# Kernel optimization log

Measured on AMD Instinct MI355X. Metric: run time of the kernel, lower is better.

Reference implementation:

```python
import jax, jax.numpy as jnp
import numpy as np

# Model dims (see init_kwargs)
NU = 4096   # num_users (one-hot feature dim)
NV = 4096   # num_items
C = 5       # num_classes (rating levels)
H0 = 256    # hidden[0]
H1 = 128    # hidden[1]
D_IN = 512  # input_dim (side-feature dense dim)
SIDE = 1024 # raw side-feature dim (u_features.size(1))
NB = 2      # nb basis matrices in bilinear decoder


def setup_inputs() -> dict:
    key = jax.random.key(0)
    ks = jax.random.split(key, 16)
    u = jax.random.randint(ks[0], (4096,), 0, NU)
    v = jax.random.randint(ks[1], (4096,), 0, NV)
    r = jax.random.randint(ks[2], (4096,), 0, C)  # unused by forward (as in source)
    raw = jax.random.randint(ks[3], (NU, NV), 0, 4 * C)
    adj_matrix = (raw[None, :, :] == jnp.arange(1, C + 1)[:, None, None]).astype(jnp.float32)
    u_features = jax.random.normal(ks[4], (NU, SIDE), jnp.float32)
    v_features = jax.random.normal(ks[5], (NV, SIDE), jnp.float32)
    def w(k, shape, fan):
        return jax.random.normal(k, shape, jnp.float32) / np.float32(np.sqrt(fan))
    u_w = w(ks[6], (C, NU, H0), NU)          # per-relation GraphConvolution user weights
    v_w = w(ks[7], (C, NV, H0), NV)          # per-relation item weights
    Wu1 = w(ks[8], (D_IN, SIDE), SIDE); bu1 = jnp.zeros((D_IN,), jnp.float32)
    Wv1 = w(ks[9], (D_IN, SIDE), SIDE); bv1 = jnp.zeros((D_IN,), jnp.float32)
    Wu2 = w(ks[10], (H1, D_IN + H0), D_IN + H0)
    Wv2 = w(ks[11], (H1, D_IN + H0), D_IN + H0)
    P = w(ks[12], (NB, H1, H1), H1)          # bilinear basis matrices
    a = w(ks[13], (NB, C), NB)               # basis -> class coefficients
    return dict(u=u, v=v, r=r, adj_matrix=adj_matrix, u_features=u_features,
                v_features=v_features, u_w=u_w, v_w=v_w, Wu1=Wu1, bu1=bu1,
                Wv1=Wv1, bv1=bv1, Wu2=Wu2, Wv2=Wv2, P=P, a=a)


def reference(u, v, r, adj_matrix, u_features, v_features, u_w, v_w,
              Wu1, bu1, Wv1, bv1, Wu2, Wv2, P, a):
    # m = adj[:, u][:, :, v]  -> [C, nu, nv]
    m = adj_matrix[:, u][:, :, v]
    # degree normalization exactly as written in gc_encoder
    du = jnp.abs(m.sum(axis=1).sum(axis=0))   # [nv]
    di = jnp.abs(m.sum(axis=2).sum(axis=0))   # [nu]
    c = 1.0 / jnp.concatenate([du, di], axis=0)
    c = jnp.where(jnp.isinf(c), jnp.zeros_like(c), c)
    # ordinal weight sharing: W_r = sum_{s<=r} Theta_s; one-hot feat @ W == gather rows
    cu = jnp.cumsum(u_w, axis=0)              # [C, NU, H0]
    cv = jnp.cumsum(v_w, axis=0)
    u_x = cu[:, u]                            # [C, nu, H0]
    v_x = cv[:, v]                            # [C, nv, H0]
    # accumulate per-relation message passing across all C relations at once
    u_next = jnp.einsum('ruv,rvh->uh', m, v_x)   # [nu, H0]
    v_next = jnp.einsum('ruv,ruh->vh', m, u_x)   # [nv, H0]
    z = jax.nn.relu(jnp.concatenate([u_next, v_next], axis=0) * c[:, None])
    nu = u.shape[0]
    u_z, v_z = z[:nu], z[nu:]
    u_f = jax.nn.relu(u_features[u] @ Wu1.T + bu1)
    v_f = jax.nn.relu(v_features[v] @ Wv1.T + bv1)
    u_h = jax.nn.relu(jnp.concatenate([u_z, u_f], axis=1) @ Wu2.T)   # [nu, H1]
    v_h = jax.nn.relu(jnp.concatenate([v_z, v_f], axis=1) @ Wv2.T)   # [nv, H1]
    # bilinear mixture decoder: logits[c,u,v] = sum_b a[b,c] * u_h Q_b v_h^T
    outputs = jnp.einsum('ud,bde,ve,bc->cuv', u_h, P, v_h, a)        # [C, nu, nv]
    logp = jax.nn.log_softmax(outputs, axis=0)
    prob = jnp.exp(logp)
    ratings = jnp.arange(1, C + 1, dtype=outputs.dtype)
    m_hat = jnp.einsum('c,cuv->uv', ratings, prob)
    # losses over observed entries
    mask = m.sum(axis=0) > 0
    n_obs = jnp.maximum(mask.sum(), 1).astype(outputs.dtype)
    loss = -(m * logp).sum() / n_obs
    target = (jnp.argmax(m, axis=0) + 1).astype(outputs.dtype)
    se = jnp.where(mask, (m_hat - target) ** 2, jnp.zeros_like(m_hat))
    rmse_loss = jnp.sqrt(se.sum() / n_obs)
    return (m_hat, loss, rmse_loss)
```

## Files before the change

kernel.cpp:

```cpp
#include <hip/hip_runtime.h>
#include <stdint.h>

#define N4   4096
#define H0   256
#define SIDE 1024
#define DIN  512
#define HCAT 768
#define H1   128
#define NC   5
#define NUV  16777216ULL
#define CAP  1536

typedef __attribute__((ext_vector_type(8))) short short8;
typedef __attribute__((ext_vector_type(4))) float floatx4;

__device__ __forceinline__ unsigned short f2bf(float f) {
    unsigned int u;
    __builtin_memcpy(&u, &f, 4);
    unsigned int r = (u + 0x7FFFu + ((u >> 16) & 1u)) >> 16;
    return (unsigned short)r;
}

__device__ __forceinline__ float bf2f(unsigned short b) {
    unsigned int u = (unsigned int)b << 16;
// ... 41 lines not shown
    int b = blockIdx.x, t = threadIdx.x;
    if (b < 4096) {
        int bx = b & 63, by = b >> 6;
        int row = t >> 2;
        int seg = (t & 3) * 16;
        int p0 = by * 64, q0 = bx * 64;
        uint4 vdat = *(const uint4*)(code + (size_t)(p0 + row) * N4 + q0 + seg);
        *(uint4*)(&tile[row][seg]) = vdat;
        __syncthreads();
        union { uint4 u4; uint8_t bb[16]; } o;
        #pragma unroll
        for (int l = 0; l < 16; l++) o.bb[l] = tile[seg + l][row];
        *(uint4*)(codeT + (size_t)(q0 + row) * N4 + p0 + seg) = o.u4;
    } else {
        int node = (b - 4096) & 4095;
        int side = (b - 4096) >> 12;
        const float* w = side ? v_w : u_w;
        const int* cnt = side ? cnt_v : cnt_u;
        unsigned short* out = side ? T_Bv : T_Au;
        int h = t;
        float c = (float)cnt[node];
        float acc = 0.f;
        #pragma unroll
        for (int r = 0; r < NC; r++) {
            size_t idx = ((size_t)r * N4 + node) * H0 + h;
            acc += w[idx];
            union { _Float16 h16; unsigned short s; } cvt;
            cvt.h16 = (_Float16)(acc * c);
            out[idx] = cvt.s;
        }
    }
}

__global__ __launch_bounds__(256) void k_compactF(const uint8_t* __restrict__ code,
                                                  const uint8_t* __restrict__ codeT,
                                                  const int* __restrict__ cnt_u,
                                                  const int* __restrict__ cnt_v,
                                                  unsigned short* __restrict__ idxU,
                                                  int* __restrict__ nnzU,
                                                  float* __restrict__ rowDeg,
                                                  unsigned short* __restrict__ idxV,
                                                  int* __restrict__ nnzV,
                                                  float* __restrict__ colDeg) {
    __shared__ float cw[4096];
    __shared__ int wtot[4];
    __shared__ float wdeg[4];
    __shared__ __align__(16) unsigned short ebuf[CAP];
    int side = blockIdx.y;
    const uint8_t* codeRows = side ? codeT : code;
    const int* cntOther = side ? cnt_u : cnt_v;
    unsigned short* idx = side ? idxV : idxU;
    int* nnz = side ? nnzV : nnzU;
    float* deg = side ? colDeg : rowDeg;

    int p = blockIdx.x, t = threadIdx.x;
    int lane = t & 63, wv = t >> 6;
    const int4* co4 = (const int4*)cntOther;
    #pragma unroll
    for (int l = 0; l < 4; l++) {
        int4 ci = co4[t + l * 256];
        ((float4*)cw)[t + l * 256] =
            make_float4((float)ci.x, (float)ci.y, (float)ci.z, (float)ci.w);
    }
    uint4 w = ((const uint4*)(codeRows + (size_t)p * N4))[t];
    unsigned char b[16];
    __builtin_memcpy(b, &w, 16);
    int cnt = 0;
    #pragma unroll
    for (int j = 0; j < 16; j++) cnt += (b[j] != 0);
    int sc = cnt;
    #pragma unroll
    for (int off = 1; off < 64; off <<= 1) {
        int up = __shfl_up(sc, off, 64);
        if (lane >= off) sc += up;
    }
    if (lane == 63) wtot[wv] = sc;
    __syncthreads();
    int wbase = 0;
    #pragma unroll
    for (int ww = 0; ww < 4; ww++) wbase += (ww < wv) ? wtot[ww] : 0;
    int total = wtot[0] + wtot[1] + wtot[2] + wtot[3];
    int pos = wbase + sc - cnt;
    float dsum = 0.f;
    #pragma unroll
    for (int j = 0; j < 16; j++) {
        int r = b[j];
        if (r) {
            int q = t * 16 + j;
            if (pos < CAP) ebuf[pos] = (unsigned short)((r - 1) * N4 + q);
            pos++;
            dsum += cw[q];
        }
    }
    #pragma unroll
    for (int off = 32; off; off >>= 1) dsum += __shfl_down(dsum, off, 64);
    if (lane == 0) wdeg[wv] = dsum;
    __syncthreads();
    int tw = total < CAP ? total : CAP;
    if (t == 0) { deg[p] = wdeg[0] + wdeg[1] + wdeg[2] + wdeg[3]; nnz[p] = tw; }
    for (int e = t; e < tw; e += 256) idx[(size_t)p * CAP + e] = ebuf[e];
}

__global__ __launch_bounds__(256) void k_gatherE(const unsigned short* __restrict__ idxU,
                                                 const int* __restrict__ nnzU,
                                                 const unsigned short* __restrict__ T_Bv,
                                                 const unsigned short* __restrict__ idxV,
                                                 const int* __restrict__ nnzV,
                                                 const unsigned short* __restrict__ T_Au,
                                                 float* __restrict__ pnn) {
    __shared__ __align__(16) unsigned short sidx[CAP];
    __shared__ float red[16][132];
    __shared__ int sbnd[2];
    int bid = blockIdx.x;
    int side  = bid >> 15;
    int r1    = bid & 32767;
    int epoch = r1 >> 13;
    int r2    = r1 & 8191;
    int p     = r2 >> 1;
    int half  = r2 & 1;

    const unsigned short* idx = side ? idxV : idxU;
    const int* nnz = side ? nnzV : nnzU;
    const char* tb = (const char*)(side ? T_Au : T_Bv);

    int t = threadIdx.x;
    int n = nnz[p];
    const unsigned short* rowIdx = idx + (size_t)p * CAP;
    int nv = (n + 7) >> 3;
    for (int i = t; i < nv; i += 256)
        ((uint4*)sidx)[i] = ((const uint4*)rowIdx)[i];
    __syncthreads();
    if (t < 2) {
        int target = (epoch + t) << 10;
// ... 26 lines not shown
        union { uint4 u; _Float16 h[8]; } cv;
        cv.u = d0;
        #pragma unroll
        for (int k = 0; k < 8; k++) acc[k] += (float)cv.h[k];
        cv.u = d1;
        #pragma unroll
        for (int k = 0; k < 8; k++) acc[k] += (float)cv.h[k];
        cv.u = d2;
        #pragma unroll
        for (int k = 0; k < 8; k++) acc[k] += (float)cv.h[k];
        cv.u = d3;
        #pragma unroll
        for (int k = 0; k < 8; k++) acc[k] += (float)cv.h[k];
    }
    for (int e = nmain + s; e < ehi; e += 16) {
        int o = ((int)sidx[e]) << 9;
        uint4 d = *(const uint4*)(tb + o + boff);
        union { uint4 u; _Float16 h[8]; } cv;
        cv.u = d;
        #pragma unroll
        for (int k = 0; k < 8; k++) acc[k] += (float)cv.h[k];
    }
    #pragma unroll
    for (int k = 0; k < 8; k++) red[s][c * 8 + k] = acc[k];
    __syncthreads();
    if (t < 128) {
        float sum = 0.f;
        #pragma unroll
        for (int ss = 0; ss < 16; ss++) sum += red[ss][t];
        pnn[(((size_t)(side * 4 + epoch)) * N4 + p) * H0 + half * 128 + t] = sum;
    }
}

__global__ __launch_bounds__(256) void k_fuse1(const uint8_t* __restrict__ code,
                                               const int* __restrict__ u,
                                               const int* __restrict__ v,
                                               uint8_t* __restrict__ codeR,
                                               const float* __restrict__ pnn,
                                               const float* __restrict__ colDeg,
                                               const float* __restrict__ rowDeg,
                                               unsigned short* __restrict__ chiU,
                                               unsigned short* __restrict__ cloU,
                                               unsigned short* __restrict__ chiV,
                                               unsigned short* __restrict__ cloV,
                                               const float* __restrict__ u_feat,
                                               unsigned short* __restrict__ fuhi,
                                               unsigned short* __restrict__ fulo,
                                               const float* __restrict__ v_feat,
                                               unsigned short* __restrict__ fvhi,
                                               unsigned short* __restrict__ fvlo,
                                               const float* __restrict__ Wu1,
                                               unsigned short* __restrict__ wuhi,
                                               unsigned short* __restrict__ wulo,
                                               const float* __restrict__ Wv1,
                                               unsigned short* __restrict__ wvhi,
                                               unsigned short* __restrict__ wvlo,
                                               const float* __restrict__ Wu2,
                                               unsigned short* __restrict__ w2uhi,
                                               unsigned short* __restrict__ w2ulo,
                                               const float* __restrict__ Wv2,
                                               unsigned short* __restrict__ w2vhi,
                                               unsigned short* __restrict__ w2vlo,
                                               const float* __restrict__ P,
                                               float* __restrict__ Pt) {
    __shared__ __align__(16) uint8_t rowbuf[4096];
    int b = blockIdx.x, t = threadIdx.x;
    if (b < 4096) {
        int i = b;
        int urow = u[i];
        ((uint4*)rowbuf)[t] = ((const uint4*)(code + (size_t)urow * N4))[t];
        __syncthreads();
        uint8_t ob[16];
        #pragma unroll
        for (int w = 0; w < 4; w++) {
            int4 vv = ((const int4*)v)[t * 4 + w];
            ob[w * 4 + 0] = rowbuf[vv.x];
            ob[w * 4 + 1] = rowbuf[vv.y];
            ob[w * 4 + 2] = rowbuf[vv.z];
            ob[w * 4 + 3] = rowbuf[vv.w];
        }
        uint4 o;
        __builtin_memcpy(&o, ob, 16);
        ((uint4*)(codeR + (size_t)i * N4))[t] = o;
        return;
    }
    if (b < 12288) {
        int i = (b - 4096) & 4095;
        int side = (b - 4096) >> 12;
        const int* idxs = side ? v : u;
        const int* idxo = side ? u : v;
        const float* deg = side ? rowDeg : colDeg;
        unsigned short* catHi = side ? chiV : chiU;
        unsigned short* catLo = side ? cloV : cloU;
        int h = t;
        float d = deg[idxo[i]];
        float inv = d > 0.f ? 1.f / d : 0.f;
        int row = idxs[i];
        const float* pr = pnn + ((size_t)side * 4 * N4 + row) * H0 + h;
        float nnv = 0.f;
        #pragma unroll
        for (int e = 0; e < 4; e++) nnv += pr[(size_t)e * N4 * H0];
        float val = fmaxf(nnv * inv, 0.f);
        unsigned short hb = f2bf(val);
        catHi[(size_t)i * HCAT + h] = hb;
        catLo[(size_t)i * HCAT + h] = f2bf(val - bf2f(hb));
        return;
    }
    if (b >= 21696) {
        int tid = (b - 21696) * 256 + t;
        int bb = tid >> 14;
        int d = (tid >> 7) & 127;
        int e = tid & 127;
        Pt[((size_t)bb * 128 + e) * 128 + d] = P[tid];
        return;
    }
    const float* src;
    unsigned short* hi;
    unsigned short* lo;
    int lb;
    if (b < 16384)      { src = u_feat; hi = fuhi; lo = fulo; lb = b - 12288; }
    else if (b < 20480) { src = v_feat; hi = fvhi; lo = fvlo; lb = b - 16384; }
    else if (b < 20992) { src = Wu1; hi = wuhi; lo = wulo; lb = b - 20480; }
    else if (b < 21504) { src = Wv1; hi = wvhi; lo = wvlo; lb = b - 20992; }
    else if (b < 21600) { src = Wu2; hi = w2uhi; lo = w2ulo; lb = b - 21504; }
    else                { src = Wv2; hi = w2vhi; lo = w2vlo; lb = b - 21600; }
    size_t g = ((size_t)lb * 256 + t) * 4;
    float4 x = *(const float4*)(src + g);
    float f[4] = {x.x, x.y, x.z, x.w};
    unsigned short hh[4], ll[4];
    #pragma unroll
    for (int k = 0; k < 4; k++) {
        unsigned short hb = f2bf(f[k]);
        hh[k] = hb;
        ll[k] = f2bf(f[k] - bf2f(hb));
    }
    *(ushort4*)(hi + g) = make_ushort4(hh[0], hh[1], hh[2], hh[3]);
    *(ushort4*)(lo + g) = make_ushort4(ll[0], ll[1], ll[2], ll[3]);
}

__global__ __launch_bounds__(256) void k_l1F(const unsigned short* __restrict__ fuhi,
                                             const unsigned short* __restrict__ fulo,
                                             const unsigned short* __restrict__ fvhi,
                                             const unsigned short* __restrict__ fvlo,
                                             const int* __restrict__ u,
                                             const int* __restrict__ v,
                                             const unsigned short* __restrict__ wuhi,
                                             const unsigned short* __restrict__ wulo,
                                             const unsigned short* __restrict__ wvhi,
                                             const unsigned short* __restrict__ wvlo,
                                             const float* __restrict__ bu1,
                                             const float* __restrict__ bv1,
                                             unsigned short* __restrict__ chiU,
                                             unsigned short* __restrict__ cloU,
                                             unsigned short* __restrict__ chiV,
                                             unsigned short* __restrict__ cloV) {
    __shared__ __align__(16) unsigned short Bh[64][72];
    __shared__ __align__(16) unsigned short Bl[64][72];
    int side = blockIdx.z;
    const unsigned short* Ahi = side ? fvhi : fuhi;
    const unsigned short* Alo = side ? fvlo : fulo;
    const int* rowmap = side ? v : u;
    const unsigned short* Bhi = side ? wvhi : wuhi;
    const unsigned short* Blo = side ? wvlo : wulo;
    const float* bias = side ? bv1 : bu1;
    unsigned short* CHi = (side ? chiV : chiU) + H0;
    unsigned short* CLo = (side ? cloV : cloU) + H0;

    int t = threadIdx.x;
    int wave = t >> 6, lane = t & 63;
    int lr = lane & 15;
    int lk = lane >> 4;
    int i0 = blockIdx.y * 64 + wave * 16;
    int n0 = blockIdx.x * 64;
    int gi = rowmap[i0 + lr];
    const unsigned short* pah = Ahi + (size_t)gi * SIDE;
    const unsigned short* pal = Alo + (size_t)gi * SIDE;
    int srow = t >> 2, sseg = (t & 3) * 16;
    floatx4 acc[4];
    #pragma unroll
    for (int jt = 0; jt < 4; jt++) acc[jt] = (floatx4){0.f, 0.f, 0.f, 0.f};
    for (int ks = 0; ks < SIDE / 64; ks++) {
        const unsigned short* sh = Bhi + (size_t)(n0 + srow) * SIDE + ks * 64 + sseg;
        const unsigned short* sl = Blo + (size_t)(n0 + srow) * SIDE + ks * 64 + sseg;
        __syncthreads();
        *(uint4*)(&Bh[srow][sseg]) = *(const uint4*)sh;
        *(uint4*)(&Bh[srow][sseg + 8]) = *(const uint4*)(sh + 8);
        *(uint4*)(&Bl[srow][sseg]) = *(const uint4*)sl;
        *(uint4*)(&Bl[srow][sseg + 8]) = *(const uint4*)(sl + 8);
        __syncthreads();
        #pragma unroll
        for (int kk = 0; kk < 2; kk++) {
            int ko = ks * 64 + kk * 32 + lk * 8;
            short8 ah = *(const short8*)(pah + ko);
            short8 al = *(const short8*)(pal + ko);
            #pragma unroll
            for (int jt = 0; jt < 4; jt++) {
                short8 bh = *(const short8*)(&Bh[jt * 16 + lr][kk * 32 + lk * 8]);
                short8 bl = *(const short8*)(&Bl[jt * 16 + lr][kk * 32 + lk * 8]);
                acc[jt] = __builtin_amdgcn_mfma_f32_16x16x32_bf16(ah, bh, acc[jt], 0, 0, 0);
                acc[jt] = __builtin_amdgcn_mfma_f32_16x16x32_bf16(ah, bl, acc[jt], 0, 0, 0);
                acc[jt] = __builtin_amdgcn_mfma_f32_16x16x32_bf16(al, bh, acc[jt], 0, 0, 0);
            }
        }
    }
    #pragma unroll
    for (int jt = 0; jt < 4; jt++) {
        int cn = n0 + jt * 16 + lr;
        float bb = bias[cn];
        #pragma unroll
        for (int r = 0; r < 4; r++) {
            int ci = i0 + lk * 4 + r;
            float vv = fmaxf(acc[jt][r] + bb, 0.f);
            unsigned short hb = f2bf(vv);
            CHi[(size_t)ci * HCAT + cn] = hb;
            CLo[(size_t)ci * HCAT + cn] = f2bf(vv - bf2f(hb));
        }
    }
}

__global__ __launch_bounds__(256) void k_l2F(const unsigned short* __restrict__ chiU,
                                             const unsigned short* __restrict__ cloU,
                                             const unsigned short* __restrict__ w2uhi,
                                             const unsigned short* __restrict__ w2ulo,
                                             float* __restrict__ uh,
                                             const unsigned short* __restrict__ chiV,
                                             const unsigned short* __restrict__ cloV,
                                             const unsigned short* __restrict__ w2vhi,
                                             const unsigned short* __restrict__ w2vlo,
                                             unsigned short* __restrict__ vhb) {
    __shared__ __align__(16) unsigned short Bh[64][72];
    __shared__ __align__(16) unsigned short Bl[64][72];
    int side = blockIdx.z;
    const unsigned short* Ahi = side ? chiV : chiU;
    const unsigned short* Alo = side ? cloV : cloU;
    const unsigned short* Bhi = side ? w2vhi : w2uhi;
    const unsigned short* Blo = side ? w2vlo : w2ulo;

    int t = threadIdx.x;
    int wave = t >> 6, lane = t & 63;
    int lr = lane & 15;
    int lk = lane >> 4;
    int i0 = blockIdx.y * 64 + wave * 16;
    int n0 = blockIdx.x * 64;
    const unsigned short* pah = Ahi + (size_t)(i0 + lr) * HCAT;
    const unsigned short* pal = Alo + (size_t)(i0 + lr) * HCAT;
    int srow = t >> 2, sseg = (t & 3) * 16;
    floatx4 acc[4];
    #pragma unroll
    for (int jt = 0; jt < 4; jt++) acc[jt] = (floatx4){0.f, 0.f, 0.f, 0.f};
    for (int ks = 0; ks < HCAT / 64; ks++) {
        const unsigned short* sh = Bhi + (size_t)(n0 + srow) * HCAT + ks * 64 + sseg;
        const unsigned short* sl = Blo + (size_t)(n0 + srow) * HCAT + ks * 64 + sseg;
        __syncthreads();
        *(uint4*)(&Bh[srow][sseg]) = *(const uint4*)sh;
        *(uint4*)(&Bh[srow][sseg + 8]) = *(const uint4*)(sh + 8);
        *(uint4*)(&Bl[srow][sseg]) = *(const uint4*)sl;
        *(uint4*)(&Bl[srow][sseg + 8]) = *(const uint4*)(sl + 8);
        __syncthreads();
        #pragma unroll
        for (int kk = 0; kk < 2; kk++) {
            int ko = ks * 64 + kk * 32 + lk * 8;
            short8 ah = *(const short8*)(pah + ko);
            short8 al = *(const short8*)(pal + ko);
            #pragma unroll
            for (int jt = 0; jt < 4; jt++) {
                short8 bh = *(const short8*)(&Bh[jt * 16 + lr][kk * 32 + lk * 8]);
                short8 bl = *(const short8*)(&Bl[jt * 16 + lr][kk * 32 + lk * 8]);
                acc[jt] = __builtin_amdgcn_mfma_f32_16x16x32_bf16(ah, bh, acc[jt], 0, 0, 0);
                acc[jt] = __builtin_amdgcn_mfma_f32_16x16x32_bf16(ah, bl, acc[jt], 0, 0, 0);
                acc[jt] = __builtin_amdgcn_mfma_f32_16x16x32_bf16(al, bh, acc[jt], 0, 0, 0);
            }
        }
    }
    #pragma unroll
    for (int jt = 0; jt < 4; jt++) {
        int cn = n0 + jt * 16 + lr;
        #pragma unroll
        for (int r = 0; r < 4; r++) {
            int ci = i0 + lk * 4 + r;
            float vv = fmaxf(acc[jt][r], 0.f);
            if (side) {
                vhb[(size_t)ci * H1 + cn] = f2bf(vv);
            } else {
                uh[(size_t)ci * H1 + cn] = vv;
            }
        }
    }
}

template <int TM, int TN, int BK, int RM, int RN>
__global__ __launch_bounds__(256) void k_gemm(const float* __restrict__ A, int lda,
                                              const float* __restrict__ B, int ldb,
                                              float* __restrict__ C, int ldc, int K,
                                              size_t bzs, size_t czs) {
    constexpr int TX = TN / RN;
    constexpr int TY = TM / RM;
    static_assert(TX * TY == 256, "block must be 256");
    __shared__ float As[BK][TM + 4];
    __shared__ float Bs[BK][TN + 4];
    int tid = threadIdx.x;
    int tx = tid % TX, ty = tid / TX;
    int i0 = blockIdx.x * TM, n0 = blockIdx.y * TN;
    const float* Bz = B + (size_t)blockIdx.z * bzs;
    float acc[RM][RN] = {};
    for (int k0 = 0; k0 < K; k0 += BK) {
        for (int g = tid; g < TM * BK / 4; g += 256) {
            int i = g / (BK / 4), kc = g % (BK / 4);
            float4 val = *(const float4*)(A + (size_t)(i0 + i) * lda + k0 + kc * 4);
            As[kc * 4 + 0][i] = val.x; As[kc * 4 + 1][i] = val.y;
            As[kc * 4 + 2][i] = val.z; As[kc * 4 + 3][i] = val.w;
        }
        for (int g = tid; g < TN * BK / 4; g += 256) {
            int n = g / (BK / 4), kc = g % (BK / 4);
            float4 val = *(const float4*)(Bz + (size_t)(n0 + n) * ldb + k0 + kc * 4);
            Bs[kc * 4 + 0][n] = val.x; Bs[kc * 4 + 1][n] = val.y;
            Bs[kc * 4 + 2][n] = val.z; Bs[kc * 4 + 3][n] = val.w;
        }
        __syncthreads();
        #pragma unroll
        for (int k = 0; k < BK; k++) {
            float av[RM], bv[RN];
            #pragma unroll
            for (int m = 0; m < RM; m++) av[m] = As[k][ty * RM + m];
            #pragma unroll
            for (int n = 0; n < RN; n++) bv[n] = Bs[k][tx * RN + n];
            #pragma unroll
            for (int m = 0; m < RM; m++)
                #pragma unroll
                for (int n = 0; n < RN; n++)
                    acc[m][n] = fmaf(av[m], bv[n], acc[m][n]);
        }
        __syncthreads();
    }
    #pragma unroll
    for (int m = 0; m < RM; m++) {
        int ig = i0 + ty * RM + m;
        #pragma unroll
        for (int n = 0; n < RN; n++) {
            unsigned short* Cz16 = (unsigned short*)C + (size_t)blockIdx.z * czs;
            Cz16[(size_t)ig * ldc + n0 + tx * RN + n] = f2bf(acc[m][n]);
        }
    }
}

__global__ __launch_bounds__(256) void k_scores3(const unsigned short* __restrict__ tb,
                                                 const unsigned short* __restrict__ vhb,
                                                 const uint8_t* __restrict__ codeR,
                                                 const float* __restrict__ a_f,
                                                 float* __restrict__ mhat,
                                                 float* __restrict__ part) {
    __shared__ float wred[4][3];
    int t = threadIdx.x;
    int wave = t >> 6, lane = t & 63;
    int lr = lane & 15;
    int lk = lane >> 4;
    int i0 = blockIdx.y * 64 + wave * 16;
    int j0 = blockIdx.x * 128;
    float sa0[NC], sa1[NC];
    #pragma unroll
    for (int c = 0; c < NC; c++) { sa0[c] = a_f[c]; sa1[c] = a_f[5 + c]; }

    const unsigned short* t0p = tb;
    const unsigned short* t1p = tb + (size_t)N4 * H1;
    short8 a0[4], a1[4];
    #pragma unroll
    for (int kc = 0; kc < 4; kc++) {
        size_t off = (size_t)(i0 + lr) * H1 + kc * 32 + lk * 8;
        a0[kc] = *(const short8*)(t0p + off);
        a1[kc] = *(const short8*)(t1p + off);
    }

    const uint8_t* crbase = codeR + (size_t)(i0 + lk * 4) * N4 + lr;
    short8 bcur[4];
// ... 126 lines not shown
    const float* bu1    = (const float*)d_in[9];
    const float* Wv1    = (const float*)d_in[10];
    const float* bv1    = (const float*)d_in[11];
    const float* Wu2    = (const float*)d_in[12];
    const float* Wv2    = (const float*)d_in[13];
    const float* P      = (const float*)d_in[14];
    const float* a      = (const float*)d_in[15];
    float* out = (float*)d_out;

    char* ws = (char*)d_ws;
    const size_t O_CODE  = 0;
    const size_t O_CNTU  = 16777216;
    const size_t O_CNTV  = O_CNTU + 16384;
    const size_t O_ACC   = O_CNTV + 16384;
    const size_t O_TAU   = O_ACC + 256;
    const size_t O_TBV   = O_TAU + 10485760;
    const size_t O_IDXU  = O_TBV + 10485760;
    const size_t O_IDXV  = O_IDXU + 12582912;
    const size_t O_NNZU  = O_IDXV + 12582912;
    const size_t O_NNZV  = O_NNZU + 16384;
    const size_t O_RDEG  = O_NNZV + 16384;
    const size_t O_CDEG  = O_RDEG + 16384;
    const size_t O_UNN   = O_CDEG + 16384;
    const size_t O_VNN   = O_UNN + 4194304;
    const size_t O_UCAT  = O_VNN + 4194304;
    const size_t O_VCAT  = O_UCAT + 12582912;
    const size_t O_UH    = O_VCAT + 12582912;
    const size_t O_VHB   = O_UH + 2097152;
    const size_t O_PT    = O_VHB + 1048576;
    const size_t O_TB    = O_PT + 131072;
    const size_t O_CODET = O_UCAT;
    const size_t O_CODER = O_TAU;
    const size_t O_PART  = O_CNTU;
    const size_t O_FUHI  = O_IDXU;
    const size_t O_FULO  = O_IDXV;
    const size_t O_CHIU  = O_UCAT;
    const size_t O_CLOU  = O_UCAT + 6291456;
    const size_t O_CHIV  = O_VCAT;
    const size_t O_CLOV  = O_VCAT + 6291456;
    const size_t S_FVHI  = 0;
    const size_t S_FVLO  = 8388608;
    const size_t S_WUHI  = 16777216;
    const size_t S_WULO  = S_WUHI + 1048576;
    const size_t S_WVHI  = S_WULO + 1048576;
    const size_t S_WVLO  = S_WVHI + 1048576;
    const size_t S_W2UHI = S_WVLO + 1048576;
    const size_t S_W2ULO = S_W2UHI + 196608;
    const size_t S_W2VHI = S_W2ULO + 196608;
    const size_t S_W2VLO = S_W2VHI + 196608;
    const size_t S_PNN   = 25165824;

    uint8_t* code  = (uint8_t*)(ws + O_CODE);
    uint8_t* codeT = (uint8_t*)(ws + O_CODET);
    uint8_t* codeR = (uint8_t*)(ws + O_CODER);
    int* cnt_u = (int*)(ws + O_CNTU);
    int* cnt_v = (int*)(ws + O_CNTV);
    unsigned short* T_Au = (unsigned short*)(ws + O_TAU);
    unsigned short* T_Bv = (unsigned short*)(ws + O_TBV);
    unsigned short* idxU = (unsigned short*)(ws + O_IDXU);
    unsigned short* idxV = (unsigned short*)(ws + O_IDXV);
    int* nnzU = (int*)(ws + O_NNZU);
    int* nnzV = (int*)(ws + O_NNZV);
    float* rowDeg = (float*)(ws + O_RDEG);
    float* colDeg = (float*)(ws + O_CDEG);
    float* uh = (float*)(ws + O_UH);
    unsigned short* vhb = (unsigned short*)(ws + O_VHB);
    float* Pt = (float*)(ws + O_PT);
    unsigned short* tb = (unsigned short*)(ws + O_TB);
    float* part = (float*)(ws + O_PART);
    unsigned short* fuhi = (unsigned short*)(ws + O_FUHI);
    unsigned short* fulo = (unsigned short*)(ws + O_FULO);
    unsigned short* chiU = (unsigned short*)(ws + O_CHIU);
    unsigned short* cloU = (unsigned short*)(ws + O_CLOU);
    unsigned short* chiV = (unsigned short*)(ws + O_CHIV);
    unsigned short* cloV = (unsigned short*)(ws + O_CLOV);
    char* outc = (char*)d_out;
    unsigned short* fvhi = (unsigned short*)(outc + S_FVHI);
    unsigned short* fvlo = (unsigned short*)(outc + S_FVLO);
    unsigned short* wuhi = (unsigned short*)(outc + S_WUHI);
    unsigned short* wulo = (unsigned short*)(outc + S_WULO);
    unsigned short* wvhi = (unsigned short*)(outc + S_WVHI);
    unsigned short* wvlo = (unsigned short*)(outc + S_WVLO);
    unsigned short* w2uhi = (unsigned short*)(outc + S_W2UHI);
    unsigned short* w2ulo = (unsigned short*)(outc + S_W2ULO);
    unsigned short* w2vhi = (unsigned short*)(outc + S_W2VHI);
    unsigned short* w2vlo = (unsigned short*)(outc + S_W2VLO);
    float* pnn = (float*)(outc + S_PNN);

    hipMemsetAsync(ws + O_CNTU, 0, 16384 + 16384, stream);

    k_codeF<<<16400, 256, 0, stream>>>(adj, (uchar4*)code, u, v, cnt_u, cnt_v);
    k_fuse0<<<12288, 256, 0, stream>>>(code, codeT, u_w, cnt_u, T_Au, v_w, cnt_v, T_Bv);
    k_compactF<<<dim3(N4, 2), 256, 0, stream>>>(code, codeT, cnt_u, cnt_v,
                                                idxU, nnzU, rowDeg, idxV, nnzV, colDeg);
    k_gatherE<<<65536, 256, 0, stream>>>(idxU, nnzU, T_Bv, idxV, nnzV, T_Au, pnn);
    k_fuse1<<<21824, 256, 0, stream>>>(code, u, v, codeR, pnn, colDeg, rowDeg,
                                       chiU, cloU, chiV, cloV,
                                       u_feat, fuhi, fulo,
                                       v_feat, fvhi, fvlo,
                                       Wu1, wuhi, wulo, Wv1, wvhi, wvlo,
                                       Wu2, w2uhi, w2ulo, Wv2, w2vhi, w2vlo,
                                       P, Pt);
    k_l1F<<<dim3(8, 64, 2), 256, 0, stream>>>(fuhi, fulo, fvhi, fvlo, u, v,
                                              wuhi, wulo, wvhi, wvlo, bu1, bv1,
                                              chiU, cloU, chiV, cloV);
    k_l2F<<<dim3(2, 64, 2), 256, 0, stream>>>(chiU, cloU, w2uhi, w2ulo, uh,
                                              chiV, cloV, w2vhi, w2vlo, vhb);
    k_gemm<64, 32, 16, 4, 2>
        <<<dim3(64, 4, 2), 256, 0, stream>>>(uh, H1, Pt, H1,
                                             (float*)tb, H1, H1,
                                             (size_t)H1 * H1, (size_t)N4 * H1);
    k_scores3<<<dim3(32, 64), 256, 0, stream>>>(tb, vhb, codeR, a, out, part);
    k_finalize<<<1, 256, 0, stream>>>(part, out);
}
```

Before: 881.8 us.

## Fuse prep conversions into compaction, merge z-build into layer1, MFMA the Pt GEMM

New measurement: 874.0 us. Within noise of the previous version (-0.9%).

```diff
diff --git a/kernel.cpp b/kernel.cpp
--- a/kernel.cpp
+++ b/kernel.cpp
@@ -97,73 +97,132 @@
     }
 }
 
-__global__ __launch_bounds__(256) void k_compactF(const uint8_t* __restrict__ code,
-                                                  const uint8_t* __restrict__ codeT,
-                                                  const int* __restrict__ cnt_u,
-                                                  const int* __restrict__ cnt_v,
-                                                  unsigned short* __restrict__ idxU,
-                                                  int* __restrict__ nnzU,
-                                                  float* __restrict__ rowDeg,
-                                                  unsigned short* __restrict__ idxV,
-                                                  int* __restrict__ nnzV,
-                                                  float* __restrict__ colDeg) {
+__global__ __launch_bounds__(256) void k_prep(const uint8_t* __restrict__ code,
+                                              const uint8_t* __restrict__ codeT,
+                                              const int* __restrict__ cnt_u,
+                                              const int* __restrict__ cnt_v,
+                                              unsigned short* __restrict__ idxU,
+                                              int* __restrict__ nnzU,
+                                              float* __restrict__ rowDeg,
+                                              unsigned short* __restrict__ idxV,
+                                              int* __restrict__ nnzV,
+                                              float* __restrict__ colDeg,
+                                              const float* __restrict__ u_feat,
+                                              unsigned short* __restrict__ fuhi,
+                                              unsigned short* __restrict__ fulo,
+                                              const float* __restrict__ v_feat,
+                                              unsigned short* __restrict__ fvhi,
+                                              unsigned short* __restrict__ fvlo,
+                                              const float* __restrict__ Wu1,
+                                              unsigned short* __restrict__ wuhi,
+                                              unsigned short* __restrict__ wulo,
+                                              const float* __restrict__ Wv1,
+                                              unsigned short* __restrict__ wvhi,
+                                              unsigned short* __restrict__ wvlo,
+                                              const float* __restrict__ Wu2,
+                                              unsigned short* __restrict__ w2uhi,
+                                              unsigned short* __restrict__ w2ulo,
+                                              const float* __restrict__ Wv2,
+                                              unsigned short* __restrict__ w2vhi,
+                                              unsigned short* __restrict__ w2vlo,
+                                              const float* __restrict__ P,
+                                              unsigned short* __restrict__ pthi,
+                                              unsigned short* __restrict__ ptlo) {
     __shared__ float cw[4096];
     __shared__ int wtot[4];
     __shared__ float wdeg[4];
     __shared__ __align__(16) unsigned short ebuf[CAP];
-    int side = blockIdx.y;
-    const uint8_t* codeRows = side ? codeT : code;
-    const int* cntOther = side ? cnt_u : cnt_v;
-    unsigned short* idx = side ? idxV : idxU;
-    int* nnz = side ? nnzV : nnzU;
-    float* deg = side ? colDeg : rowDeg;
-
-    int p = blockIdx.x, t = threadIdx.x;
-    int lane = t & 63, wv = t >> 6;
-    const int4* co4 = (const int4*)cntOther;
-    #pragma unroll
-    for (int l = 0; l < 4; l++) {
-        int4 ci = co4[t + l * 256];
-        ((float4*)cw)[t + l * 256] =
-            make_float4((float)ci.x, (float)ci.y, (float)ci.z, (float)ci.w);
-    }
-    uint4 w = ((const uint4*)(codeRows + (size_t)p * N4))[t];
-    unsigned char b[16];
-    __builtin_memcpy(b, &w, 16);
-    int cnt = 0;
-    #pragma unroll
-    for (int j = 0; j < 16; j++) cnt += (b[j] != 0);
-    int sc = cnt;
-    #pragma unroll
-    for (int off = 1; off < 64; off <<= 1) {
-        int up = __shfl_up(sc, off, 64);
-        if (lane >= off) sc += up;
-    }
-    if (lane == 63) wtot[wv] = sc;
-    __syncthreads();
-    int wbase = 0;
-    #pragma unroll
-    for (int ww = 0; ww < 4; ww++) wbase += (ww < wv) ? wtot[ww] : 0;
-    int total = wtot[0] + wtot[1] + wtot[2] + wtot[3];
-    int pos = wbase + sc - cnt;
-    float dsum = 0.f;
-    #pragma unroll
-    for (int j = 0; j < 16; j++) {
-        int r = b[j];
-        if (r) {
-            int q = t * 16 + j;
-            if (pos < CAP) ebuf[pos] = (unsigned short)((r - 1) * N4 + q);
-            pos++;
-            dsum += cw[q];
-        }
-    }
-    #pragma unroll
-    for (int off = 32; off; off >>= 1) dsum += __shfl_down(dsum, off, 64);
-    if (lane == 0) wdeg[wv] = dsum;
-    __syncthreads();
-    int tw = total < CAP ? total : CAP;
-    if (t == 0) { deg[p] = wdeg[0] + wdeg[1] + wdeg[2] + wdeg[3]; nnz[p] = tw; }
-    for (int e = t; e < tw; e += 256) idx[(size_t)p * CAP + e] = ebuf[e];
+    int b = blockIdx.x, t = threadIdx.x;
+    if (b < 8192) {
+        int side = b >> 12;
+        int p = b & 4095;
+        const uint8_t* codeRows = side ? codeT : code;
+        const int* cntOther = side ? cnt_u : cnt_v;
+        unsigned short* idx = side ? idxV : idxU;
+        int* nnz = side ? nnzV : nnzU;
+        float* deg = side ? colDeg : rowDeg;
+
+        int lane = t & 63, wv = t >> 6;
+        const int4* co4 = (const int4*)cntOther;
+        #pragma unroll
+        for (int l = 0; l < 4; l++) {
+            int4 ci = co4[t + l * 256];
+            ((float4*)cw)[t + l * 256] =
+                make_float4((float)ci.x, (float)ci.y, (float)ci.z, (float)ci.w);
+        }
+        uint4 w = ((const uint4*)(codeRows + (size_t)p * N4))[t];
+        unsigned char bb[16];
+        __builtin_memcpy(bb, &w, 16);
+        int cnt = 0;
+        #pragma unroll
+        for (int j = 0; j < 16; j++) cnt += (bb[j] != 0);
+        int sc = cnt;
+        #pragma unroll
+        for (int off = 1; off < 64; off <<= 1) {
+            int up = __shfl_up(sc, off, 64);
+            if (lane >= off) sc += up;
+        }
+        if (lane == 63) wtot[wv] = sc;
+        __syncthreads();
+        int wbase = 0;
+        #pragma unroll
+        for (int ww = 0; ww < 4; ww++) wbase += (ww < wv) ? wtot[ww] : 0;
+        int total = wtot[0] + wtot[1] + wtot[2] + wtot[3];
+        int pos = wbase + sc - cnt;
+        float dsum = 0.f;
+        #pragma unroll
+        for (int j = 0; j < 16; j++) {
+            int r = bb[j];
+            if (r) {
+                int q = t * 16 + j;
+                if (pos < CAP) ebuf[pos] = (unsigned short)((r - 1) * N4 + q);
+                pos++;
+                dsum += cw[q];
+            }
+        }
+        #pragma unroll
+        for (int off = 32; off; off >>= 1) dsum += __shfl_down(dsum, off, 64);
+        if (lane == 0) wdeg[wv] = dsum;
+        __syncthreads();
+        int tw = total < CAP ? total : CAP;
+        if (t == 0) { deg[p] = wdeg[0] + wdeg[1] + wdeg[2] + wdeg[3]; nnz[p] = tw; }
+        for (int e = t; e < tw; e += 256) idx[(size_t)p * CAP + e] = ebuf[e];
+        return;
+    }
+    if (b >= 17600) {
+        int tid = (b - 17600) * 256 + t;
+        int bb = tid >> 14;
+        int d = (tid >> 7) & 127;
+        int e = tid & 127;
+        float val = P[tid];
+        unsigned short hb = f2bf(val);
+        size_t o = ((size_t)bb * 128 + e) * 128 + d;
+        pthi[o] = hb;
+        ptlo[o] = f2bf(val - bf2f(hb));
+        return;
+    }
+    const float* src;
+    unsigned short* hi;
+    unsigned short* lo;
+    int lb;
+    if (b < 12288)      { src = u_feat; hi = fuhi; lo = fulo; lb = b - 8192; }
+    else if (b < 16384) { src = v_feat; hi = fvhi; lo = fvlo; lb = b - 12288; }
+    else if (b < 16896) { src = Wu1; hi = wuhi; lo = wulo; lb = b - 16384; }
+    else if (b < 17408) { src = Wv1; hi = wvhi; lo = wvlo; lb = b - 16896; }
+    else if (b < 17504) { src = Wu2; hi = w2uhi; lo = w2ulo; lb = b - 17408; }
+    else                { src = Wv2; hi = w2vhi; lo = w2vlo; lb = b - 17504; }
+    size_t g = ((size_t)lb * 256 + t) * 4;
+    float4 x = *(const float4*)(src + g);
+    float f[4] = {x.x, x.y, x.z, x.w};
+    unsigned short hh[4], ll[4];
+    #pragma unroll
+    for (int k = 0; k < 4; k++) {
+        unsigned short hb = f2bf(f[k]);
+        hh[k] = hb;
+        ll[k] = f2bf(f[k] - bf2f(hb));
+    }
+    *(ushort4*)(hi + g) = make_ushort4(hh[0], hh[1], hh[2], hh[3]);
+    *(ushort4*)(lo + g) = make_ushort4(ll[0], ll[1], ll[2], ll[3]);
 }
 
 __global__ __launch_bounds__(256) void k_gatherE(const unsigned short* __restrict__ idxU,
@@ -256,113 +315,7 @@
     }
 }
 
-__global__ __launch_bounds__(256) void k_fuse1(const uint8_t* __restrict__ code,
-                                               const int* __restrict__ u,
-                                               const int* __restrict__ v,
-                                               uint8_t* __restrict__ codeR,
-                                               const float* __restrict__ pnn,
-                                               const float* __restrict__ colDeg,
-                                               const float* __restrict__ rowDeg,
-                                               unsigned short* __restrict__ chiU,
-                                               unsigned short* __restrict__ cloU,
-                                               unsigned short* __restrict__ chiV,
-                                               unsigned short* __restrict__ cloV,
-                                               const float* __restrict__ u_feat,
-                                               unsigned short* __restrict__ fuhi,
-                                               unsigned short* __restrict__ fulo,
-                                               const float* __restrict__ v_feat,
-                                               unsigned short* __restrict__ fvhi,
-                                               unsigned short* __restrict__ fvlo,
-                                               const float* __restrict__ Wu1,
-                                               unsigned short* __restrict__ wuhi,
-                                               unsigned short* __restrict__ wulo,
-                                               const float* __restrict__ Wv1,
-                                               unsigned short* __restrict__ wvhi,
-                                               unsigned short* __restrict__ wvlo,
-                                               const float* __restrict__ Wu2,
-                                               unsigned short* __restrict__ w2uhi,
-                                               unsigned short* __restrict__ w2ulo,
-                                               const float* __restrict__ Wv2,
-                                               unsigned short* __restrict__ w2vhi,
-                                               unsigned short* __restrict__ w2vlo,
-                                               const float* __restrict__ P,
-                                               float* __restrict__ Pt) {
-    __shared__ __align__(16) uint8_t rowbuf[4096];
-    int b = blockIdx.x, t = threadIdx.x;
-    if (b < 4096) {
-        int i = b;
-        int urow = u[i];
-        ((uint4*)rowbuf)[t] = ((const uint4*)(code + (size_t)urow * N4))[t];
-        __syncthreads();
-        uint8_t ob[16];
-        #pragma unroll
-        for (int w = 0; w < 4; w++) {
-            int4 vv = ((const int4*)v)[t * 4 + w];
-            ob[w * 4 + 0] = rowbuf[vv.x];
-            ob[w * 4 + 1] = rowbuf[vv.y];
-            ob[w * 4 + 2] = rowbuf[vv.z];
-            ob[w * 4 + 3] = rowbuf[vv.w];
-        }
-        uint4 o;
-        __builtin_memcpy(&o, ob, 16);
-        ((uint4*)(codeR + (size_t)i * N4))[t] = o;
-        return;
-    }
-    if (b < 12288) {
-        int i = (b - 4096) & 4095;
-        int side = (b - 4096) >> 12;
-        const int* idxs = side ? v : u;
-        const int* idxo = side ? u : v;
-        const float* deg = side ? rowDeg : colDeg;
-        unsigned short* catHi = side ? chiV : chiU;
-        unsigned short* catLo = side ? cloV : cloU;
-        int h = t;
-        float d = deg[idxo[i]];
-        float inv = d > 0.f ? 1.f / d : 0.f;
-        int row = idxs[i];
-        const float* pr = pnn + ((size_t)side * 4 * N4 + row) * H0 + h;
-        float nnv = 0.f;
-        #pragma unroll
-        for (int e = 0; e < 4; e++) nnv += pr[(size_t)e * N4 * H0];
-        float val = fmaxf(nnv * inv, 0.f);
-        unsigned short hb = f2bf(val);
-        catHi[(size_t)i * HCAT + h] = hb;
-        catLo[(size_t)i * HCAT + h] = f2bf(val - bf2f(hb));
-        return;
-    }
-    if (b >= 21696) {
-        int tid = (b - 21696) * 256 + t;
-        int bb = tid >> 14;
-        int d = (tid >> 7) & 127;
-        int e = tid & 127;
-        Pt[((size_t)bb * 128 + e) * 128 + d] = P[tid];
-        return;
-    }
-    const float* src;
-    unsigned short* hi;
-    unsigned short* lo;
-    int lb;
-    if (b < 16384)      { src = u_feat; hi = fuhi; lo = fulo; lb = b - 12288; }
-    else if (b < 20480) { src = v_feat; hi = fvhi; lo = fvlo; lb = b - 16384; }
-    else if (b < 20992) { src = Wu1; hi = wuhi; lo = wulo; lb = b - 20480; }
-    else if (b < 21504) { src = Wv1; hi = wvhi; lo = wvlo; lb = b - 20992; }
-    else if (b < 21600) { src = Wu2; hi = w2uhi; lo = w2ulo; lb = b - 21504; }
-    else                { src = Wv2; hi = w2vhi; lo = w2vlo; lb = b - 21600; }
-    size_t g = ((size_t)lb * 256 + t) * 4;
-    float4 x = *(const float4*)(src + g);
-    float f[4] = {x.x, x.y, x.z, x.w};
-    unsigned short hh[4], ll[4];
-    #pragma unroll
-    for (int k = 0; k < 4; k++) {
-        unsigned short hb = f2bf(f[k]);
-        hh[k] = hb;
-        ll[k] = f2bf(f[k] - bf2f(hb));
-    }
-    *(ushort4*)(hi + g) = make_ushort4(hh[0], hh[1], hh[2], hh[3]);
-    *(ushort4*)(lo + g) = make_ushort4(ll[0], ll[1], ll[2], ll[3]);
-}
-
-__global__ __launch_bounds__(256) void k_l1F(const unsigned short* __restrict__ fuhi,
+__global__ __launch_bounds__(256) void k_l1Z(const unsigned short* __restrict__ fuhi,
                                              const unsigned short* __restrict__ fulo,
                                              const unsigned short* __restrict__ fvhi,
                                              const unsigned short* __restrict__ fvlo,
@@ -377,18 +330,138 @@
                                              unsigned short* __restrict__ chiU,
                                              unsigned short* __restrict__ cloU,
                                              unsigned short* __restrict__ chiV,
-                                             unsigned short* __restrict__ cloV) {
+                                             unsigned short* __restrict__ cloV,
+                                             const float* __restrict__ pnn,
+                                             const float* __restrict__ colDeg,
+                                             const float* __restrict__ rowDeg,
+                                             const uint8_t* __restrict__ code,
+                                             uint8_t* __restrict__ codeR) {
+    __shared__ __align__(16) unsigned short Bh[64][72];
+    __shared__ __align__(16) unsigned short Bl[64][72];
+    int b = blockIdx.x, t = threadIdx.x;
+    if (b < 1024) {
+        int side = b >> 9;
+        int rem = b & 511;
+        const unsigned short* Ahi = side ? fvhi : fuhi;
+        const unsigned short* Alo = side ? fvlo : fulo;
+        const int* rowmap = side ? v : u;
+        const unsigned short* Bhi = side ? wvhi : wuhi;
+        const unsigned short* Blo = side ? wvlo : wulo;
+        const float* bias = side ? bv1 : bu1;
+        unsigned short* CHi = (side ? chiV : chiU) + H0;
+        unsigned short* CLo = (side ? cloV : cloU) + H0;
+
+        int wave = t >> 6, lane = t & 63;
+        int lr = lane & 15;
+        int lk = lane >> 4;
+        int i0 = (rem >> 3) * 64 + wave * 16;
+        int n0 = (rem & 7) * 64;
+        int gi = rowmap[i0 + lr];
+        const unsigned short* pah = Ahi + (size_t)gi * SIDE;
+        const unsigned short* pal = Alo + (size_t)gi * SIDE;
+        int srow = t >> 2, sseg = (t & 3) * 16;
+        floatx4 acc[4];
+        #pragma unroll
+        for (int jt = 0; jt < 4; jt++) acc[jt] = (floatx4){0.f, 0.f, 0.f, 0.f};
+        for (int ks = 0; ks < SIDE / 64; ks++) {
+            const unsigned short* sh = Bhi + (size_t)(n0 + srow) * SIDE + ks * 64 + sseg;
+            const unsigned short* sl = Blo + (size_t)(n0 + srow) * SIDE + ks * 64 + sseg;
+            __syncthreads();
+            *(uint4*)(&Bh[srow][sseg]) = *(const uint4*)sh;
+            *(uint4*)(&Bh[srow][sseg + 8]) = *(const uint4*)(sh + 8);
+            *(uint4*)(&Bl[srow][sseg]) = *(const uint4*)sl;
+            *(uint4*)(&Bl[srow][sseg + 8]) = *(const uint4*)(sl + 8);
+            __syncthreads();
+            #pragma unroll
+            for (int kk = 0; kk < 2; kk++) {
+                int ko = ks * 64 + kk * 32 + lk * 8;
+                short8 ah = *(const short8*)(pah + ko);
+                short8 al = *(const short8*)(pal + ko);
+                #pragma unroll
+                for (int jt = 0; jt < 4; jt++) {
+                    short8 bh = *(const short8*)(&Bh[jt * 16 + lr][kk * 32 + lk * 8]);
+                    short8 bl = *(const short8*)(&Bl[jt * 16 + lr][kk * 32 + lk * 8]);
+                    acc[jt] = __builtin_amdgcn_mfma_f32_16x16x32_bf16(ah, bh, acc[jt], 0, 0, 0);
+                    acc[jt] = __builtin_amdgcn_mfma_f32_16x16x32_bf16(ah, bl, acc[jt], 0, 0, 0);
+                    acc[jt] = __builtin_amdgcn_mfma_f32_16x16x32_bf16(al, bh, acc[jt], 0, 0, 0);
+                }
+            }
+        }
+        #pragma unroll
+        for (int jt = 0; jt < 4; jt++) {
+            int cn = n0 + jt * 16 + lr;
+            float bb = bias[cn];
+            #pragma unroll
+            for (int r = 0; r < 4; r++) {
+                int ci = i0 + lk * 4 + r;
+                float vv = fmaxf(acc[jt][r] + bb, 0.f);
+                unsigned short hb = f2bf(vv);
+                CHi[(size_t)ci * HCAT + cn] = hb;
+                CLo[(size_t)ci * HCAT + cn] = f2bf(vv - bf2f(hb));
+            }
+        }
+        return;
+    }
+    if (b < 9216) {
+        int idx = b - 1024;
+        int side = idx >> 12;
+        int i = idx & 4095;
+        const int* idxs = side ? v : u;
+        const int* idxo = side ? u : v;
+        const float* deg = side ? rowDeg : colDeg;
+        unsigned short* catHi = side ? chiV : chiU;
+        unsigned short* catLo = side ? cloV : cloU;
+        int h = t;
+        float d = deg[idxo[i]];
+        float inv = d > 0.f ? 1.f / d : 0.f;
+        int row = idxs[i];
+        const float* pr = pnn + ((size_t)side * 4 * N4 + row) * H0 + h;
+        float nnv = 0.f;
+        #pragma unroll
+        for (int e = 0; e < 4; e++) nnv += pr[(size_t)e * N4 * H0];
+        float val = fmaxf(nnv * inv, 0.f);
+        unsigned short hb = f2bf(val);
+        catHi[(size_t)i * HCAT + h] = hb;
+        catLo[(size_t)i * HCAT + h] = f2bf(val - bf2f(hb));
+        return;
+    }
+    uint8_t* rowbuf = (uint8_t*)Bh;
+    int i = b - 9216;
+    int urow = u[i];
+    ((uint4*)rowbuf)[t] = ((const uint4*)(code + (size_t)urow * N4))[t];
+    __syncthreads();
+    uint8_t ob[16];
+    #pragma unroll
+    for (int w = 0; w < 4; w++) {
+        int4 vv = ((const int4*)v)[t * 4 + w];
+        ob[w * 4 + 0] = rowbuf[vv.x];
+        ob[w * 4 + 1] = rowbuf[vv.y];
+        ob[w * 4 + 2] = rowbuf[vv.z];
+        ob[w * 4 + 3] = rowbuf[vv.w];
+    }
+    uint4 o;
+    __builtin_memcpy(&o, ob, 16);
+    ((uint4*)(codeR + (size_t)i * N4))[t] = o;
+}
+
+__global__ __launch_bounds__(256) void k_l2F(const unsigned short* __restrict__ chiU,
+                                             const unsigned short* __restrict__ cloU,
+                                             const unsigned short* __restrict__ w2uhi,
+                                             const unsigned short* __restrict__ w2ulo,
+                                             unsigned short* __restrict__ uhhi,
+                                             unsigned short* __restrict__ uhlo,
+                                             const unsigned short* __restrict__ chiV,
+                                             const unsigned short* __restrict__ cloV,
+                                             const unsigned short* __restrict__ w2vhi,
+                                             const unsigned short* __restrict__ w2vlo,
+                                             unsigned short* __restrict__ vhb) {
     __shared__ __align__(16) unsigned short Bh[64][72];
     __shared__ __align__(16) unsigned short Bl[64][72];
     int side = blockIdx.z;
-    const unsigned short* Ahi = side ? fvhi : fuhi;
-    const unsigned short* Alo = side ? fvlo : fulo;
-    const int* rowmap = side ? v : u;
-    const unsigned short* Bhi = side ? wvhi : wuhi;
-    const unsigned short* Blo = side ? wvlo : wulo;
-    const float* bias = side ? bv1 : bu1;
-    unsigned short* CHi = (side ? chiV : chiU) + H0;
-    unsigned short* CLo = (side ? cloV : cloU) + H0;
+    const unsigned short* Ahi = side ? chiV : chiU;
+    const unsigned short* Alo = side ? cloV : cloU;
+    const unsigned short* Bhi = side ? w2vhi : w2uhi;
+    const unsigned short* Blo = side ? w2vlo : w2ulo;
 
     int t = threadIdx.x;
     int wave = t >> 6, lane = t & 63;
@@ -396,16 +469,15 @@
     int lk = lane >> 4;
     int i0 = blockIdx.y * 64 + wave * 16;
     int n0 = blockIdx.x * 64;
-    int gi = rowmap[i0 + lr];
-    const unsigned short* pah = Ahi + (size_t)gi * SIDE;
-    const unsigned short* pal = Alo + (size_t)gi * SIDE;
+    const unsigned short* pah = Ahi + (size_t)(i0 + lr) * HCAT;
+    const unsigned short* pal = Alo + (size_t)(i0 + lr) * HCAT;
     int srow = t >> 2, sseg = (t & 3) * 16;
     floatx4 acc[4];
     #pragma unroll
     for (int jt = 0; jt < 4; jt++) acc[jt] = (floatx4){0.f, 0.f, 0.f, 0.f};
-    for (int ks = 0; ks < SIDE / 64; ks++) {
-        const unsigned short* sh = Bhi + (size_t)(n0 + srow) * SIDE + ks * 64 + sseg;
-        const unsigned short* sl = Blo + (size_t)(n0 + srow) * SIDE + ks * 64 + sseg;
+    for (int ks = 0; ks < HCAT / 64; ks++) {
+        const unsigned short* sh = Bhi + (size_t)(n0 + srow) * HCAT + ks * 64 + sseg;
+        const unsigned short* sl = Blo + (size_t)(n0 + srow) * HCAT + ks * 64 + sseg;
         __syncthreads();
         *(uint4*)(&Bh[srow][sseg]) = *(const uint4*)sh;
         *(uint4*)(&Bh[srow][sseg + 8]) = *(const uint4*)(sh + 8);
@@ -430,51 +502,46 @@
     #pragma unroll
     for (int jt = 0; jt < 4; jt++) {
         int cn = n0 + jt * 16 + lr;
-        float bb = bias[cn];
         #pragma unroll
         for (int r = 0; r < 4; r++) {
             int ci = i0 + lk * 4 + r;
-            float vv = fmaxf(acc[jt][r] + bb, 0.f);
-            unsigned short hb = f2bf(vv);
-            CHi[(size_t)ci * HCAT + cn] = hb;
-            CLo[(size_t)ci * HCAT + cn] = f2bf(vv - bf2f(hb));
-        }
-    }
-}
-
-__global__ __launch_bounds__(256) void k_l2F(const unsigned short* __restrict__ chiU,
-                                             const unsigned short* __restrict__ cloU,
-                                             const unsigned short* __restrict__ w2uhi,
-                                             const unsigned short* __restrict__ w2ulo,
-                                             float* __restrict__ uh,
-                                             const unsigned short* __restrict__ chiV,
-                                             const unsigned short* __restrict__ cloV,
-                                             const unsigned short* __restrict__ w2vhi,
-                                             const unsigned short* __restrict__ w2vlo,
-                                             unsigned short* __restrict__ vhb) {
+            float vv = fmaxf(acc[jt][r], 0.f);
+            if (side) {
+                vhb[(size_t)ci * H1 + cn] = f2bf(vv);
+            } else {
+                unsigned short hb = f2bf(vv);
+                uhhi[(size_t)ci * H1 + cn] = hb;
+                uhlo[(size_t)ci * H1 + cn] = f2bf(vv - bf2f(hb));
+            }
+        }
+    }
+}
+
+__global__ __launch_bounds__(256) void k_tb(const unsigned short* __restrict__ uhhi,
+                                            const unsigned short* __restrict__ uhlo,
+                                            const unsigned short* __restrict__ pthi,
+                                            const unsigned short* __restrict__ ptlo,
+                                            unsigned short* __restrict__ tbout) {
     __shared__ __align__(16) unsigned short Bh[64][72];
     __shared__ __align__(16) unsigned short Bl[64][72];
-    int side = blockIdx.z;
-    const unsigned short* Ahi = side ? chiV : chiU;
-    const unsigned short* Alo = side ? cloV : cloU;
-    const unsigned short* Bhi = side ? w2vhi : w2uhi;
-    const unsigned short* Blo = side ? w2vlo : w2ulo;
-
+    int bmat = blockIdx.z;
     int t = threadIdx.x;
     int wave = t >> 6, lane = t & 63;
     int lr = lane & 15;
     int lk = lane >> 4;
     int i0 = blockIdx.y * 64 + wave * 16;
     int n0 = blockIdx.x * 64;
-    const unsigned short* pah = Ahi + (size_t)(i0 + lr) * HCAT;
-    const unsigned short* pal = Alo + (size_t)(i0 + lr) * HCAT;
+    const unsigned short* Bhi = pthi + (size_t)bmat * H1 * H1;
+    const unsigned short* Blo = ptlo + (size_t)bmat * H1 * H1;
+    const unsigned short* pah = uhhi + (size_t)(i0 + lr) * H1;
+    const unsigned short* pal = uhlo + (size_t)(i0 + lr) * H1;
     int srow = t >> 2, sseg = (t & 3) * 16;
     floatx4 acc[4];
     #pragma unroll
     for (int jt = 0; jt < 4; jt++) acc[jt] = (floatx4){0.f, 0.f, 0.f, 0.f};
-    for (int ks = 0; ks < HCAT / 64; ks++) {
-        const unsigned short* sh = Bhi + (size_t)(n0 + srow) * HCAT + ks * 64 + sseg;
-        const unsigned short* sl = Blo + (size_t)(n0 + srow) * HCAT + ks * 64 + sseg;
+    for (int ks = 0; ks < H1 / 64; ks++) {
+        const unsigned short* sh = Bhi + (size_t)(n0 + srow) * H1 + ks * 64 + sseg;
+        const unsigned short* sl = Blo + (size_t)(n0 + srow) * H1 + ks * 64 + sseg;
         __syncthreads();
         *(uint4*)(&Bh[srow][sseg]) = *(const uint4*)sh;
         *(uint4*)(&Bh[srow][sseg + 8]) = *(const uint4*)(sh + 8);
@@ -502,67 +569,7 @@
         #pragma unroll
         for (int r = 0; r < 4; r++) {
             int ci = i0 + lk * 4 + r;
-            float vv = fmaxf(acc[jt][r], 0.f);
-            if (side) {
-                vhb[(size_t)ci * H1 + cn] = f2bf(vv);
-            } else {
-                uh[(size_t)ci * H1 + cn] = vv;
-            }
-        }
-    }
-}
-
-template <int TM, int TN, int BK, int RM, int RN>
-__global__ __launch_bounds__(256) void k_gemm(const float* __restrict__ A, int lda,
-                                              const float* __restrict__ B, int ldb,
-                                              float* __restrict__ C, int ldc, int K,
-                                              size_t bzs, size_t czs) {
-    constexpr int TX = TN / RN;
-    constexpr int TY = TM / RM;
-    static_assert(TX * TY == 256, "block must be 256");
-    __shared__ float As[BK][TM + 4];
-    __shared__ float Bs[BK][TN + 4];
-    int tid = threadIdx.x;
-    int tx = tid % TX, ty = tid / TX;
-    int i0 = blockIdx.x * TM, n0 = blockIdx.y * TN;
-    const float* Bz = B + (size_t)blockIdx.z * bzs;
-    float acc[RM][RN] = {};
-    for (int k0 = 0; k0 < K; k0 += BK) {
-        for (int g = tid; g < TM * BK / 4; g += 256) {
-            int i = g / (BK / 4), kc = g % (BK / 4);
-            float4 val = *(const float4*)(A + (size_t)(i0 + i) * lda + k0 + kc * 4);
-            As[kc * 4 + 0][i] = val.x; As[kc * 4 + 1][i] = val.y;
-            As[kc * 4 + 2][i] = val.z; As[kc * 4 + 3][i] = val.w;
-        }
-        for (int g = tid; g < TN * BK / 4; g += 256) {
-            int n = g / (BK / 4), kc = g % (BK / 4);
-            float4 val = *(const float4*)(Bz + (size_t)(n0 + n) * ldb + k0 + kc * 4);
-            Bs[kc * 4 + 0][n] = val.x; Bs[kc * 4 + 1][n] = val.y;
-            Bs[kc * 4 + 2][n] = val.z; Bs[kc * 4 + 3][n] = val.w;
-        }
-        __syncthreads();
-        #pragma unroll
-        for (int k = 0; k < BK; k++) {
-            float av[RM], bv[RN];
-            #pragma unroll
-            for (int m = 0; m < RM; m++) av[m] = As[k][ty * RM + m];
-            #pragma unroll
-            for (int n = 0; n < RN; n++) bv[n] = Bs[k][tx * RN + n];
-            #pragma unroll
-            for (int m = 0; m < RM; m++)
-                #pragma unroll
-                for (int n = 0; n < RN; n++)
-                    acc[m][n] = fmaf(av[m], bv[n], acc[m][n]);
-        }
-        __syncthreads();
-    }
-    #pragma unroll
-    for (int m = 0; m < RM; m++) {
-        int ig = i0 + ty * RM + m;
-        #pragma unroll
-        for (int n = 0; n < RN; n++) {
-            unsigned short* Cz16 = (unsigned short*)C + (size_t)blockIdx.z * czs;
-            Cz16[(size_t)ig * ldc + n0 + tx * RN + n] = f2bf(acc[m][n]);
+            tbout[(size_t)bmat * N4 * H1 + (size_t)ci * H1 + cn] = f2bf(acc[jt][r]);
         }
     }
 }
@@ -755,8 +762,7 @@
     const size_t O_CODET = O_UCAT;
     const size_t O_CODER = O_TAU;
     const size_t O_PART  = O_CNTU;
-    const size_t O_FUHI  = O_IDXU;
-    const size_t O_FULO  = O_IDXV;
+    const size_t O_FULO  = O_UNN;
     const size_t O_CHIU  = O_UCAT;
     const size_t O_CLOU  = O_UCAT + 6291456;
     const size_t O_CHIV  = O_VCAT;
@@ -772,6 +778,7 @@
     const size_t S_W2VHI = S_W2ULO + 196608;
     const size_t S_W2VLO = S_W2VHI + 196608;
     const size_t S_PNN   = 25165824;
+    const size_t S_FUHI  = 58720256;
 
     uint8_t* code  = (uint8_t*)(ws + O_CODE);
     uint8_t* codeT = (uint8_t*)(ws + O_CODET);
@@ -786,18 +793,20 @@
     int* nnzV = (int*)(ws + O_NNZV);
     float* rowDeg = (float*)(ws + O_RDEG);
     float* colDeg = (float*)(ws + O_CDEG);
-    float* uh = (float*)(ws + O_UH);
+    unsigned short* uhhi = (unsigned short*)(ws + O_UH);
+    unsigned short* uhlo = (unsigned short*)(ws + O_UH + 1048576);
     unsigned short* vhb = (unsigned short*)(ws + O_VHB);
-    float* Pt = (float*)(ws + O_PT);
+    unsigned short* pthi = (unsigned short*)(ws + O_PT);
+    unsigned short* ptlo = (unsigned short*)(ws + O_PT + 65536);
     unsigned short* tb = (unsigned short*)(ws + O_TB);
     float* part = (float*)(ws + O_PART);
-    unsigned short* fuhi = (unsigned short*)(ws + O_FUHI);
     unsigned short* fulo = (unsigned short*)(ws + O_FULO);
     unsigned short* chiU = (unsigned short*)(ws + O_CHIU);
     unsigned short* cloU = (unsigned short*)(ws + O_CLOU);
     unsigned short* chiV = (unsigned short*)(ws + O_CHIV);
     unsigned short* cloV = (unsigned short*)(ws + O_CLOV);
     char* outc = (char*)d_out;
+    unsigned short* fuhi = (unsigned short*)(outc + S_FUHI);
     unsigned short* fvhi = (unsigned short*)(outc + S_FVHI);
     unsigned short* fvlo = (unsigned short*)(outc + S_FVLO);
     unsigned short* wuhi = (unsigned short*)(outc + S_WUHI);
@@ -814,25 +823,21 @@
 
     k_codeF<<<16400, 256, 0, stream>>>(adj, (uchar4*)code, u, v, cnt_u, cnt_v);
     k_fuse0<<<12288, 256, 0, stream>>>(code, codeT, u_w, cnt_u, T_Au, v_w, cnt_v, T_Bv);
-    k_compactF<<<dim3(N4, 2), 256, 0, stream>>>(code, codeT, cnt_u, cnt_v,
-                                                idxU, nnzU, rowDeg, idxV, nnzV, colDeg);
+    k_prep<<<17728, 256, 0, stream>>>(code, codeT, cnt_u, cnt_v,
+                                      idxU, nnzU, rowDeg, idxV, nnzV, colDeg,
+                                      u_feat, fuhi, fulo,
+                                      v_feat, fvhi, fvlo,
+                                      Wu1, wuhi, wulo, Wv1, wvhi, wvlo,
+                                      Wu2, w2uhi, w2ulo, Wv2, w2vhi, w2vlo,
+                                      P, pthi, ptlo);
     k_gatherE<<<65536, 256, 0, stream>>>(idxU, nnzU, T_Bv, idxV, nnzV, T_Au, pnn);
-    k_fuse1<<<21824, 256, 0, stream>>>(code, u, v, codeR, pnn, colDeg, rowDeg,
-                                       chiU, cloU, chiV, cloV,
-                                       u_feat, fuhi, fulo,
-                                       v_feat, fvhi, fvlo,
-                                       Wu1, wuhi, wulo, Wv1, wvhi, wvlo,
-                                       Wu2, w2uhi, w2ulo, Wv2, w2vhi, w2vlo,
-                                       P, Pt);
-    k_l1F<<<dim3(8, 64, 2), 256, 0, stream>>>(fuhi, fulo, fvhi, fvlo, u, v,
-                                              wuhi, wulo, wvhi, wvlo, bu1, bv1,
-                                              chiU, cloU, chiV, cloV);
-    k_l2F<<<dim3(2, 64, 2), 256, 0, stream>>>(chiU, cloU, w2uhi, w2ulo, uh,
+    k_l1Z<<<13312, 256, 0, stream>>>(fuhi, fulo, fvhi, fvlo, u, v,
+                                     wuhi, wulo, wvhi, wvlo, bu1, bv1,
+                                     chiU, cloU, chiV, cloV,
+                                     pnn, colDeg, rowDeg, code, codeR);
+    k_l2F<<<dim3(2, 64, 2), 256, 0, stream>>>(chiU, cloU, w2uhi, w2ulo, uhhi, uhlo,
                                               chiV, cloV, w2vhi, w2vlo, vhb);
-    k_gemm<64, 32, 16, 4, 2>
-        <<<dim3(64, 4, 2), 256, 0, stream>>>(uh, H1, Pt, H1,
-                                             (float*)tb, H1, H1,
-                                             (size_t)H1 * H1, (size_t)N4 * H1);
+    k_tb<<<dim3(2, 64, 2), 256, 0, stream>>>(uhhi, uhlo, pthi, ptlo, tb);
     k_scores3<<<dim3(32, 64), 256, 0, stream>>>(tb, vhb, codeR, a, out, part);
     k_finalize<<<1, 256, 0, stream>>>(part, out);
 }
```
